# Kernel optimization log

Measured on AMD Instinct MI355X. Metric: run time of the kernel, lower is better.

The kernel has to match this reference:

```python
import jax, jax.numpy as jnp
import numpy as np

N, FIN, NH, NR, F, E = 50000, 256, 4, 4, 64, 500000


def setup_inputs() -> dict:
    key = jax.random.key(0)
    ks = jax.random.split(key, 12)
    x = jax.random.normal(ks[0], (N, FIN), jnp.float32)
    src = jax.random.randint(ks[1], (E,), 0, N)
    trg = jax.random.randint(ks[2], (E,), 0, N)
    rel = jax.random.randint(ks[3], (E,), 0, NR)
    node_to_graph_map = jnp.zeros((N,), jnp.int32)
    s = 1.0 / np.sqrt(FIN)
    W_proj = jax.random.uniform(ks[4], (NH * NR * F, FIN), jnp.float32, -s, s)
    score_src = jax.random.normal(ks[5], (1, NH, NR, F), jnp.float32) * 0.1
    score_trg = jax.random.normal(ks[6], (1, NH, NR, F), jnp.float32) * 0.1
    sf = 1.0 / np.sqrt(F)
    W1 = jax.random.uniform(ks[7], (F, F), jnp.float32, -sf, sf)
    b1 = jnp.zeros((F,), jnp.float32)
    W2 = jax.random.uniform(ks[8], (F, F), jnp.float32, -sf, sf)
    b2 = jnp.zeros((F,), jnp.float32)
    W3 = jax.random.uniform(ks[9], (1, F), jnp.float32, -sf, sf)
    b3 = jnp.zeros((1,), jnp.float32)
    W_skip = jax.random.uniform(ks[10], (NH * F, FIN), jnp.float32, -s, s)
    bias = jnp.zeros((NH * F,), jnp.float32)
    gamma = jnp.ones((NH * F,), jnp.float32)
    beta = jnp.zeros((NH * F,), jnp.float32)
    return dict(x=x, src=src, trg=trg, rel=rel, node_to_graph_map=node_to_graph_map,
                W_proj=W_proj, score_src=score_src, score_trg=score_trg,
                W1=W1, b1=b1, W2=W2, b2=b2, W3=W3, b3=b3,
                W_skip=W_skip, bias=bias, gamma=gamma, beta=beta)


def mish(v):
    return v * jnp.tanh(jax.nn.softplus(v))


def gat_forward(x, W_proj, score_src, score_trg, W1, b1, W2, b2, W3, b3,
                W_skip, bias, gamma, beta, src, trg, rel):
    n = x.shape[0]
    # (N, NH, NR, F) projected node features
    proj = (x @ W_proj.T).reshape(n, NH, NR, F)
    s_src = (proj * score_src).sum(-1)  # (N, NH, NR)
    s_trg = (proj * score_trg).sum(-1)  # (N, NH, NR)
    # lift to edges for their own relation: (E, NH)
    e_s = s_src[src, :, rel] + s_trg[trg, :, rel]
    e_s = jax.nn.leaky_relu(e_s, 0.2)
    # per-(relation, head) max over edges (matches per-relation max(dim=0) in the torch loop)
    m = jax.ops.segment_max(e_s, rel, num_segments=NR)  # (NR, NH)
    e_exp = jnp.exp(e_s - m[rel])
    # segment softmax grouped by (target node, relation)
    seg = trg * NR + rel
    denom = jax.ops.segment_sum(e_exp, seg, num_segments=n * NR)  # (N*NR, NH)
    att = e_exp / (denom[seg] + 1e-16)  # (E, NH)
    feat = proj[src, :, rel, :] * att[:, :, None]  # (E, NH, F)
    agg = jax.ops.segment_sum(feat, seg, num_segments=n * NR)  # (N*NR, NH, F)
    agg = agg.reshape(n, NR, NH, F).transpose(0, 2, 1, 3)  # (N, NH, NR, F)
    # AttentionedAggregationLayer: MLP score -> Mish -> softmax over relation dim -> weighted sum
    h = jax.nn.relu(agg @ W1.T + b1)
    h = jax.nn.relu(h @ W2.T + b2)
    sc = mish(h @ W3.T + b3)            # (N, NH, NR, 1)
    a_rel = jax.nn.softmax(sc, axis=-2)
    out = (agg * a_rel).sum(-2)          # (N, NH, F)
    # skip connection (FIN != NH*F per-head, so projected skip), concat heads, bias, ELU, LayerNorm
    out = out + (x @ W_skip.T).reshape(n, NH, F)
    out = out.reshape(n, NH * F) + bias
    out = jax.nn.elu(out)
    mu = out.mean(-1, keepdims=True)
    var = out.var(-1, keepdims=True)
    out = (out - mu) * jax.lax.rsqrt(var + 1e-5) * gamma + beta
    return out


def reference(x, src, trg, rel, node_to_graph_map, W_proj, score_src, score_trg,
              W1, b1, W2, b2, W3, b3, W_skip, bias, gamma, beta):
    return gat_forward(x, W_proj, score_src, score_trg, W1, b1, W2, b2, W3, b3,
                       W_skip, bias, gamma, beta, src, trg, rel)
```

## Files before the change

### kernel.cpp

```cpp
#include <hip/hip_runtime.h>

#define NNODES 50000
#define NEDGES 500000
#define NBINS  (NNODES * 4)
#define NSCANB 196
#define MPAD   50176

#define WF_W1    0
#define WF_B1    4096
#define WF_W2    4160
#define WF_B2    8256
#define WF_W3    8320
#define WF_B3    8384
#define WF_SSC   8388
#define WF_STC   9412
#define WF_BIAS  10436
#define WF_GAMMA 10692
#define WF_BETA  10948
#define WF_TOT   11204
#define WB_TOT   8192

typedef __attribute__((ext_vector_type(8))) short short8;
typedef __attribute__((ext_vector_type(4))) short short4v;
typedef __attribute__((ext_vector_type(4))) float floatx4;
typedef __attribute__((ext_vector_type(4))) unsigned int uint4v;

__device__ __forceinline__ float bf2f(unsigned short u) {
    return __uint_as_float(((unsigned)u) << 16);
}
__device__ __forceinline__ unsigned f2bf(float f) {
    unsigned u = __float_as_uint(f);
    u += 0x7fffu + ((u >> 16) & 1u);
    return u >> 16;
}
__device__ __forceinline__ int clampi(int v, int hi) { return v < 0 ? 0 : (v > hi ? hi : v); }

__global__ __launch_bounds__(256) void probe_k(const unsigned short* __restrict__ xs,
                                               unsigned* __restrict__ flag) {
    __shared__ unsigned cnt;
    if (threadIdx.x == 0) cnt = 0;
    __syncthreads();
    unsigned local = 0;
    for (int i = threadIdx.x; i < 8192; i += 256) {
        float v = bf2f(xs[i]);
        if (!(fabsf(v) < 1e10f)) local++;
    }
    atomicAdd(&cnt, local);
    __syncthreads();
    if (threadIdx.x == 0) *flag = (cnt > 256u) ? 1u : 0u;
}

__device__ __forceinline__ float ldf(const void* p, int i, bool f32) {
    return f32 ? ((const float*)p)[i] : bf2f(((const unsigned short*)p)[i]);
}

__global__ __launch_bounds__(1024) void wconv_k(const void* W1, const void* b1,
                                                const void* W2, const void* b2,
                                                const void* W3, const void* b3,
                                                const void* ssc, const void* stc,
                                                const void* bias, const void* gamma,
                                                const void* beta,
                                                const unsigned* __restrict__ flag,
                                                float* __restrict__ wf,
                                                unsigned short* __restrict__ wbf16) {
    bool f32 = (*flag != 0u);
    for (int i = threadIdx.x; i < WF_TOT + WB_TOT; i += 1024) {
        if (i >= WF_TOT) {
            int j = i - WF_TOT;
            float v = (j < 4096) ? ldf(W1, j, f32) : ldf(W2, j - 4096, f32);
            wbf16[j] = (unsigned short)f2bf(v);
            continue;
        }
        float v;
        if (i < WF_B1)          v = ldf(W1, i - WF_W1, f32);
        else if (i < WF_W2)     v = ldf(b1, i - WF_B1, f32);
        else if (i < WF_B2)     v = ldf(W2, i - WF_W2, f32);
        else if (i < WF_W3)     v = ldf(b2, i - WF_B2, f32);
        else if (i < WF_B3)     v = ldf(W3, i - WF_W3, f32);
        else if (i < WF_SSC) {
            int j = i - WF_B3;
            v = (j < 1) ? ldf(b3, j, f32) : 0.f;
        }
        else if (i < WF_STC)    v = ldf(ssc, i - WF_SSC, f32);
        else if (i < WF_BIAS)   v = ldf(stc, i - WF_STC, f32);
        else if (i < WF_GAMMA)  v = ldf(bias, i - WF_BIAS, f32);
        else if (i < WF_BETA)   v = ldf(gamma, i - WF_GAMMA, f32);
        else                    v = ldf(beta, i - WF_BETA, f32);
        wf[i] = v;
    }
}

__global__ __launch_bounds__(256) void convbf_k(const void* __restrict__ src,
                                                unsigned short* __restrict__ dst,
                                                int nelem, int npad,
                                                const unsigned* __restrict__ flag) {
    int i8 = (blockIdx.x * 256 + threadIdx.x) * 8;
    if (i8 >= npad) return;
    short8 o;
    if (i8 < nelem) {
        if (*flag) {
            const float* pf = (const float*)src + i8;
            floatx4 a = *(const floatx4*)pf;
            floatx4 b = *(const floatx4*)(pf + 4);
            o[0] = (short)f2bf(a[0]); o[1] = (short)f2bf(a[1]);
            o[2] = (short)f2bf(a[2]); o[3] = (short)f2bf(a[3]);
            o[4] = (short)f2bf(b[0]); o[5] = (short)f2bf(b[1]);
            o[6] = (short)f2bf(b[2]); o[7] = (short)f2bf(b[3]);
        } else {
            o = *(const short8*)((const unsigned short*)src + i8);
        }
    } else {
#pragma unroll
        for (int j = 0; j < 8; j++) o[j] = 0;
    }
    *(short8*)(dst + i8) = o;
}

__global__ __launch_bounds__(64) void gemm_fused_k(const unsigned short* __restrict__ A,
                                                   const unsigned short* __restrict__ Bp,
                                                   const unsigned short* __restrict__ Bs,
                                                   unsigned short* __restrict__ proj,
                                                   unsigned short* __restrict__ out16,
                                                   float* __restrict__ out32,
                                                   const float* __restrict__ wf,
                                                   float* __restrict__ s_src,
                                                   float* __restrict__ s_trg,
                                                   const unsigned* __restrict__ flag) {
    const bool cf32 = (*flag != 0u);
    const int lane = threadIdx.x & 63;
    const int l15 = lane & 15, q = lane >> 4;
    const int m0 = blockIdx.x * 64;
    const int cg0 = blockIdx.y * 4;

    short8 af[4][8];
#pragma unroll
    for (int mt = 0; mt < 4; mt++)
#pragma unroll
        for (int ks = 0; ks < 8; ks++)
            af[mt][ks] = *(const short8*)(A + (size_t)(m0 + mt * 16 + l15) * 256 + ks * 32 + q * 8);

    if (cg0 < 16) {
#pragma unroll 1
        for (int cgi = 0; cgi < 4; cgi++) {
            const int cg = cg0 + cgi;
            floatx4 acc[4][4];
#pragma unroll
            for (int i = 0; i < 4; i++)
#pragma unroll
                for (int j = 0; j < 4; j++) acc[i][j] = (floatx4){0.f, 0.f, 0.f, 0.f};
#pragma unroll
            for (int ks = 0; ks < 8; ks++) {
                short8 bfr[4];
#pragma unroll
                for (int nt = 0; nt < 4; nt++)
                    bfr[nt] = *(const short8*)(Bp + (size_t)(cg * 64 + nt * 16 + l15) * 256 + ks * 32 + q * 8);
#pragma unroll
                for (int mt = 0; mt < 4; mt++)
#pragma unroll
                    for (int nt = 0; nt < 4; nt++)
                        acc[mt][nt] = __builtin_amdgcn_mfma_f32_16x16x32_bf16(bfr[nt], af[mt][ks],
                                                                             acc[mt][nt], 0, 0, 0);
            }
            const int h = cg >> 2, r = cg & 3;
            const int colbase = (r * 4 + h) * 64;
            const int cell = r * 4 + h;
            const int scell = h * 4 + r;
            floatx4 sa4[4], sb4[4];
#pragma unroll
            for (int nt = 0; nt < 4; nt++) {
                sa4[nt] = *(const floatx4*)(wf + WF_SSC + scell * 64 + nt * 16 + q * 4);
                sb4[nt] = *(const floatx4*)(wf + WF_STC + scell * 64 + nt * 16 + q * 4);
            }
#pragma unroll
            for (int mt = 0; mt < 4; mt++) {
                const int row = m0 + mt * 16 + l15;
                float pa = 0.f, pb = 0.f;
#pragma unroll
                for (int nt = 0; nt < 4; nt++) {
                    short4v sv;
#pragma unroll
                    for (int rg = 0; rg < 4; rg++) {
                        float v = acc[mt][nt][rg];
                        unsigned short vb = (unsigned short)f2bf(v);
                        sv[rg] = (short)vb;
                        float vr = bf2f(vb);
                        pa = fmaf(vr, sa4[nt][rg], pa);
                        pb = fmaf(vr, sb4[nt][rg], pb);
                    }
                    if (row < NNODES)
                        *(short4v*)(proj + (size_t)row * 1024 + colbase + nt * 16 + q * 4) = sv;
                }
                pa += __shfl_xor(pa, 16);
                pa += __shfl_xor(pa, 32);
                pb += __shfl_xor(pb, 16);
                pb += __shfl_xor(pb, 32);
                if (q == 0 && row < NNODES) {
                    s_src[row * 16 + cell] = pa;
                    s_trg[row * 16 + cell] = pb;
                }
            }
        }
    } else {
#pragma unroll 1
        for (int cg = 0; cg < 4; cg++) {
            floatx4 acc[4][4];
#pragma unroll
            for (int i = 0; i < 4; i++)
#pragma unroll
                for (int j = 0; j < 4; j++) acc[i][j] = (floatx4){0.f, 0.f, 0.f, 0.f};
#pragma unroll
            for (int ks = 0; ks < 8; ks++) {
                short8 bfr[4];
#pragma unroll
                for (int nt = 0; nt < 4; nt++)
                    bfr[nt] = *(const short8*)(Bs + (size_t)(cg * 64 + nt * 16 + l15) * 256 + ks * 32 + q * 8);
#pragma unroll
                for (int mt = 0; mt < 4; mt++)
#pragma unroll
                    for (int nt = 0; nt < 4; nt++)
                        acc[mt][nt] = __builtin_amdgcn_mfma_f32_16x16x32_bf16(bfr[nt], af[mt][ks],
                                                                             acc[mt][nt], 0, 0, 0);
            }
#pragma unroll
            for (int mt = 0; mt < 4; mt++) {
                const int row = m0 + mt * 16 + l15;
                if (row >= NNODES) continue;
#pragma unroll
                for (int nt = 0; nt < 4; nt++) {
                    if (cf32) {
                        floatx4 o = acc[mt][nt];
                        *(floatx4*)(out32 + (size_t)row * 256 + cg * 64 + nt * 16 + q * 4) = o;
                    } else {
                        short4v sv;
#pragma unroll
                        for (int rg = 0; rg < 4; rg++)
                            sv[rg] = (short)f2bf(acc[mt][nt][rg]);
                        *(short4v*)(out16 + (size_t)row * 256 + cg * 64 + nt * 16 + q * 4) = sv;
                    }
                }
            }
        }
    }
}

__global__ __launch_bounds__(256) void count_k(const int* __restrict__ trg,
                                               const int* __restrict__ rel,
                                               unsigned* __restrict__ counts, int E) {
    int e = blockIdx.x * 256 + threadIdx.x;
    if (e >= E) return;
    int g = clampi(trg[e], NNODES - 1);
    int r = clampi(rel[e], 3);
    atomicAdd(&counts[g * 4 + r], 1u);
}

__global__ __launch_bounds__(256) void scan1_k(const unsigned* __restrict__ counts,
                                               unsigned* __restrict__ offsets,
                                               unsigned* __restrict__ bsum) {
    __shared__ unsigned ts[256];
    int t = threadIdx.x;
    int base = blockIdx.x * 1024 + t * 4;
    uint4v c = {0u, 0u, 0u, 0u};
    if (base + 3 < NBINS) c = *(const uint4v*)(counts + base);
    else {
#pragma unroll
        for (int j = 0; j < 4; j++) c[j] = (base + j < NBINS) ? counts[base + j] : 0u;
    }
    ts[t] = c[0] + c[1] + c[2] + c[3];
    __syncthreads();
    for (int off = 1; off < 256; off <<= 1) {
        unsigned v = (t >= off) ? ts[t - off] : 0u;
        __syncthreads();
        ts[t] += v;
        __syncthreads();
    }
    unsigned pre = (t == 0) ? 0u : ts[t - 1];
    uint4v o;
    o[0] = pre;
    o[1] = pre + c[0];
    o[2] = pre + c[0] + c[1];
    o[3] = pre + c[0] + c[1] + c[2];
    if (base + 3 < NBINS) *(uint4v*)(offsets + base) = o;
    else {
#pragma unroll
        for (int j = 0; j < 4; j++) if (base + j < NBINS) offsets[base + j] = o[j];
    }
    if (t == 255) bsum[blockIdx.x] = ts[255];
}

__global__ __launch_bounds__(256) void scan2_k(unsigned* __restrict__ bsum,
                                               unsigned* __restrict__ offsets) {
    __shared__ unsigned ts[256];
    int t = threadIdx.x;
    unsigned v = (t < NSCANB) ? bsum[t] : 0u;
    ts[t] = v;
    __syncthreads();
    for (int off = 1; off < 256; off <<= 1) {
        unsigned u = (t >= off) ? ts[t - off] : 0u;
        __syncthreads();
        ts[t] += u;
        __syncthreads();
    }
    if (t < NSCANB) bsum[t] = (t == 0) ? 0u : ts[t - 1];
    if (t == 255) offsets[NBINS] = ts[255];
}

__global__ __launch_bounds__(256) void scan3_k(unsigned* __restrict__ offsets,
                                               unsigned* __restrict__ cursor,
                                               const unsigned* __restrict__ bsum) {
    int t = threadIdx.x;
    unsigned base = bsum[blockIdx.x];
    int idx = blockIdx.x * 1024 + t * 4;
    if (idx + 3 < NBINS) {
        uint4v o = *(const uint4v*)(offsets + idx);
        o[0] += base; o[1] += base; o[2] += base; o[3] += base;
        *(uint4v*)(offsets + idx) = o;
        *(uint4v*)(cursor + idx) = o;
    } else {
#pragma unroll
        for (int j = 0; j < 4; j++)
            if (idx + j < NBINS) {
                unsigned v = offsets[idx + j] + base;
                offsets[idx + j] = v;
                cursor[idx + j] = v;
            }
    }
}

__global__ __launch_bounds__(256) void fill_k(const int* __restrict__ src,
                                              const int* __restrict__ trg,
                                              const int* __restrict__ rel,
                                              const float* __restrict__ s_src,
                                              const float* __restrict__ s_trg,
                                              unsigned* __restrict__ cursor,
                                              unsigned* __restrict__ esrc,
                                              floatx4* __restrict__ eexp, int E) {
    int e = blockIdx.x * 256 + threadIdx.x;
    if (e >= E) return;
    int s = clampi(src[e], NNODES - 1);
    int g = clampi(trg[e], NNODES - 1);
    int r = clampi(rel[e], 3);
    unsigned pos = atomicAdd(&cursor[g * 4 + r], 1u);
    if (pos >= (unsigned)E) pos = E - 1;
    esrc[pos] = (unsigned)s;
    floatx4 aa = *(const floatx4*)(s_src + s * 16 + r * 4);
    floatx4 bb = *(const floatx4*)(s_trg + g * 16 + r * 4);
    floatx4 v;
#pragma unroll
    for (int h = 0; h < 4; h++) {
        float val = aa[h] + bb[h];
        val = val > 0.f ? val : 0.2f * val;
        v[h] = expf(val);
    }
    eexp[pos] = v;
}

__device__ __forceinline__ void edge_acc(const unsigned* esrc, const floatx4* eexp,
                                         const unsigned short* proj, int r, int h,
                                         int lane, unsigned beg, unsigned end,
                                         float* a, float* den) {
    unsigned i = beg;
    for (; i + 2 <= end; i += 2) {
        unsigned s0 = esrc[i], s1 = esrc[i + 1];
        floatx4 pe0 = eexp[i], pe1 = eexp[i + 1];
        short4v v0 = *((const short4v*)(proj + (size_t)s0 * 1024 + r * 256) + lane);
        short4v v1 = *((const short4v*)(proj + (size_t)s1 * 1024 + r * 256) + lane);
        float p0 = pe0[h], p1 = pe1[h];
        *den += p0 + p1;
        a[0] = fmaf(p0, bf2f((unsigned short)v0[0]), a[0]);
        a[1] = fmaf(p0, bf2f((unsigned short)v0[1]), a[1]);
        a[2] = fmaf(p0, bf2f((unsigned short)v0[2]), a[2]);
        a[3] = fmaf(p0, bf2f((unsigned short)v0[3]), a[3]);
        a[0] = fmaf(p1, bf2f((unsigned short)v1[0]), a[0]);
        a[1] = fmaf(p1, bf2f((unsigned short)v1[1]), a[1]);
        a[2] = fmaf(p1, bf2f((unsigned short)v1[2]), a[2]);
        a[3] = fmaf(p1, bf2f((unsigned short)v1[3]), a[3]);
    }
    if (i < end) {
        unsigned s0 = esrc[i];
        floatx4 pe0 = eexp[i];
        short4v v0 = *((const short4v*)(proj + (size_t)s0 * 1024 + r * 256) + lane);
        float p0 = pe0[h];
        *den += p0;
        a[0] = fmaf(p0, bf2f((unsigned short)v0[0]), a[0]);
        a[1] = fmaf(p0, bf2f((unsigned short)v0[1]), a[1]);
        a[2] = fmaf(p0, bf2f((unsigned short)v0[2]), a[2]);
        a[3] = fmaf(p0, bf2f((unsigned short)v0[3]), a[3]);
    }
}

__global__ __launch_bounds__(256) void node_fused_k(const unsigned* __restrict__ offsets,
                                                    const unsigned* __restrict__ esrc,
                                                    const floatx4* __restrict__ eexp,
                                                    const unsigned short* __restrict__ proj,
                                                    const unsigned short* __restrict__ wbf16,
                                                    const float* __restrict__ wf,
                                                    const unsigned* __restrict__ flag,
                                                    unsigned short* __restrict__ out16,
                                                    float* __restrict__ out32) {
    __shared__ unsigned short aggL[4][16 * 72];
    __shared__ float hidL[4][16 * 68];
    const bool f32 = (*flag != 0u);
    const int wave = threadIdx.x >> 6;
    const int lane = threadIdx.x & 63;
    const int l15 = lane & 15, q = lane >> 4;
    unsigned short* aL = aggL[wave];
    float* hL = hidL[wave];

    short8 w1f[2][4], w2f[2][4];
#pragma unroll
    for (int ks = 0; ks < 2; ks++)
#pragma unroll
        for (int nt = 0; nt < 4; nt++) {
            w1f[ks][nt] = *(const short8*)(wbf16 + (nt * 16 + l15) * 64 + ks * 32 + q * 8);
            w2f[ks][nt] = *(const short8*)(wbf16 + 4096 + (nt * 16 + l15) * 64 + ks * 32 + q * 8);
        }
    float b1v[4], b2v[4], w3v[4];
#pragma unroll
    for (int nt = 0; nt < 4; nt++) {
        b1v[nt] = wf[WF_B1 + nt * 16 + l15];
        b2v[nt] = wf[WF_B2 + nt * 16 + l15];
        w3v[nt] = wf[WF_W3 + nt * 16 + l15];
    }
    const float b3v = wf[WF_B3];

    const int c0 = q * 64 + l15 * 4;
    const floatx4 bi = *(const floatx4*)(wf + WF_BIAS + c0);
    const floatx4 ga = *(const floatx4*)(wf + WF_GAMMA + c0);
    const floatx4 be = *(const floatx4*)(wf + WF_BETA + c0);

    const int n = blockIdx.x * 4 + wave;

#pragma unroll
    for (int r = 0; r < 4; r++) {
        const int bin = n * 4 + r;
        unsigned beg = offsets[bin], end = offsets[bin + 1];
        float a[4] = {0.f, 0.f, 0.f, 0.f};
        float den = 0.f;
        edge_acc(esrc, eexp, proj, r, q, lane, beg, end, a, &den);
        float inv = 1.f / (den + 1e-16f);
        short4v o;
        o[0] = (short)f2bf(a[0] * inv);
        o[1] = (short)f2bf(a[1] * inv);
        o[2] = (short)f2bf(a[2] * inv);
        o[3] = (short)f2bf(a[3] * inv);
        *(short4v*)(aL + (r * 4 + q) * 72 + l15 * 4) = o;
    }

    short8 a1[2];
#pragma unroll
    for (int ks = 0; ks < 2; ks++)
        a1[ks] = *(const short8*)(aL + l15 * 72 + ks * 32 + q * 8);
    floatx4 acc1[4];
#pragma unroll
    for (int nt = 0; nt < 4; nt++) {
        acc1[nt] = (floatx4){0.f, 0.f, 0.f, 0.f};
        acc1[nt] = __builtin_amdgcn_mfma_f32_16x16x32_bf16(a1[0], w1f[0][nt], acc1[nt], 0, 0, 0);
        acc1[nt] = __builtin_amdgcn_mfma_f32_16x16x32_bf16(a1[1], w1f[1][nt], acc1[nt], 0, 0, 0);
    }
#pragma unroll
    for (int nt = 0; nt < 4; nt++)
#pragma unroll
        for (int rg = 0; rg < 4; rg++)
            hL[(q * 4 + rg) * 68 + nt * 16 + l15] = fmaxf(acc1[nt][rg] + b1v[nt], 0.f);
    short8 a2[2];
#pragma unroll
    for (int ks = 0; ks < 2; ks++) {
        short8 rr;
#pragma unroll
        for (int j = 0; j < 8; j++)
            rr[j] = (short)f2bf(hL[l15 * 68 + ks * 32 + q * 8 + j]);
        a2[ks] = rr;
    }
    floatx4 acc2[4];
#pragma unroll
    for (int nt = 0; nt < 4; nt++) {
        acc2[nt] = (floatx4){0.f, 0.f, 0.f, 0.f};
        acc2[nt] = __builtin_amdgcn_mfma_f32_16x16x32_bf16(a2[0], w2f[0][nt], acc2[nt], 0, 0, 0);
        acc2[nt] = __builtin_amdgcn_mfma_f32_16x16x32_bf16(a2[1], w2f[1][nt], acc2[nt], 0, 0, 0);
    }
    float p[4];
#pragma unroll
    for (int rg = 0; rg < 4; rg++) {
        float s = 0.f;
#pragma unroll
        for (int nt = 0; nt < 4; nt++)
            s = fmaf(fmaxf(acc2[nt][rg] + b2v[nt], 0.f), w3v[nt], s);
        p[rg] = s;
    }
#pragma unroll
    for (int off = 1; off < 16; off <<= 1) {
#pragma unroll
        for (int rg = 0; rg < 4; rg++) p[rg] += __shfl_xor(p[rg], off);
    }
    float psel = (l15 & 2) ? ((l15 & 1) ? p[3] : p[2])
                           : ((l15 & 1) ? p[1] : p[0]);
    float acc = psel + b3v;
    float sp = fmaxf(acc, 0.f) + log1pf(expf(-fabsf(acc)));
    float msh = acc * tanhf(sp);

    float sv0 = __shfl(msh, 0 * 16 + q);
    float sv1 = __shfl(msh, 1 * 16 + q);
    float sv2 = __shfl(msh, 2 * 16 + q);
    float sv3 = __shfl(msh, 3 * 16 + q);
    float mx = fmaxf(fmaxf(sv0, sv1), fmaxf(sv2, sv3));
    float e0 = expf(sv0 - mx), e1 = expf(sv1 - mx);
    float e2 = expf(sv2 - mx), e3 = expf(sv3 - mx);
    float inv = 1.f / (e0 + e1 + e2 + e3);
    float er[4] = {e0 * inv, e1 * inv, e2 * inv, e3 * inv};

    float acc4[4] = {0.f, 0.f, 0.f, 0.f};
#pragma unroll
    for (int r = 0; r < 4; r++) {
        short4v av = *(const short4v*)(aL + (r * 4 + q) * 72 + l15 * 4);
        float e = er[r];
        acc4[0] = fmaf(e, bf2f((unsigned short)av[0]), acc4[0]);
        acc4[1] = fmaf(e, bf2f((unsigned short)av[1]), acc4[1]);
        acc4[2] = fmaf(e, bf2f((unsigned short)av[2]), acc4[2]);
        acc4[3] = fmaf(e, bf2f((unsigned short)av[3]), acc4[3]);
    }

    const size_t ob = (size_t)n * 256 + c0;
    float v[4];
    if (f32) {
        floatx4 sk = *(const floatx4*)(out32 + ob);
#pragma unroll
        for (int j = 0; j < 4; j++) v[j] = acc4[j] + sk[j] + bi[j];
    } else {
        short4v sk = *(const short4v*)(out16 + ob);
#pragma unroll
        for (int j = 0; j < 4; j++) v[j] = acc4[j] + bf2f((unsigned short)sk[j]) + bi[j];
    }
#pragma unroll
    for (int j = 0; j < 4; j++) v[j] = v[j] > 0.f ? v[j] : expm1f(v[j]);

    float s = v[0] + v[1] + v[2] + v[3];
    float qq = v[0] * v[0] + v[1] * v[1] + v[2] * v[2] + v[3] * v[3];
#pragma unroll
    for (int o = 1; o < 64; o <<= 1) {
        s += __shfl_xor(s, o);
        qq += __shfl_xor(qq, o);
    }
    float mu = s * (1.f / 256.f);
    float var = fmaxf(qq * (1.f / 256.f) - mu * mu, 0.f);
    float rstd = rsqrtf(var + 1e-5f);

    if (f32) {
        floatx4 o4v;
#pragma unroll
        for (int j = 0; j < 4; j++) o4v[j] = (v[j] - mu) * rstd * ga[j] + be[j];
        *(floatx4*)(out32 + ob) = o4v;
    } else {
        short4v o4v;
#pragma unroll
        for (int j = 0; j < 4; j++) o4v[j] = (short)f2bf((v[j] - mu) * rstd * ga[j] + be[j]);
        *(short4v*)(out16 + ob) = o4v;
    }
}

extern "C" void kernel_launch(void* const* d_in, const int* in_sizes, int n_in,
                              void* d_out, int out_size, void* d_ws, size_t ws_size,
                              hipStream_t stream) {
    if (ws_size < 226900000) return;

    const void* x      = d_in[0];
    const int* src     = (const int*)d_in[1];
    const int* trg     = (const int*)d_in[2];
    const int* rel     = (const int*)d_in[3];
    const void* W_proj = d_in[5];
    const void* ssc    = d_in[6];
    const void* stc    = d_in[7];
    const void* W1     = d_in[8];
    const void* b1     = d_in[9];
    const void* W2     = d_in[10];
    const void* b2     = d_in[11];
    const void* W3     = d_in[12];
    const void* b3     = d_in[13];
    const void* W_skip = d_in[14];
    const void* bias   = d_in[15];
    const void* gamma  = d_in[16];
    const void* beta   = d_in[17];
    unsigned short* out16 = (unsigned short*)d_out;
    float* out32          = (float*)d_out;

    char* w = (char*)d_ws;
    unsigned short* proj = (unsigned short*)(w + 0);
    unsigned short* xbf  = (unsigned short*)(w + 102400000);
    float* s_src         = (float*)(w + 204800000);
    float* s_trg         = (float*)(w + 208000000);
    floatx4* eexp        = (floatx4*)(w + 211200000);
    unsigned short* wpbf = (unsigned short*)(w + 211200000);
    unsigned short* wsbf = (unsigned short*)(w + 212300000);
    unsigned* esrc       = (unsigned*)(w + 219200000);
    unsigned* counts     = (unsigned*)(w + 221200000);
    unsigned* offsets    = (unsigned*)(w + 222000000);
    unsigned* cursor     = (unsigned*)(w + 222800016);
    float* wf            = (float*)(w + 226800016);
    unsigned short* wbf16= (unsigned short*)(w + 226844832);
    unsigned* flag       = (unsigned*)(w + 226861216);
    unsigned* bsum       = (unsigned*)(w + 226861224);

    hipMemsetAsync(counts, 0, NBINS * 4, stream);

    probe_k<<<1, 256, 0, stream>>>((const unsigned short*)x, flag);
    wconv_k<<<1, 1024, 0, stream>>>(W1, b1, W2, b2, W3, b3, ssc, stc, bias, gamma, beta,
                                    flag, wf, wbf16);
    convbf_k<<<(MPAD * 256) / (8 * 256), 256, 0, stream>>>(x, xbf, NNODES * 256,
                                                           MPAD * 256, flag);
    convbf_k<<<128, 256, 0, stream>>>(W_proj, wpbf, 1024 * 256, 1024 * 256, flag);
    convbf_k<<<32, 256, 0, stream>>>(W_skip, wsbf, 256 * 256, 256 * 256, flag);
    gemm_fused_k<<<dim3(784, 5), 64, 0, stream>>>(xbf, wpbf, wsbf, proj, out16, out32,
                                                  wf, s_src, s_trg, flag);
    count_k<<<1954, 256, 0, stream>>>(trg, rel, counts, NEDGES);
    scan1_k<<<NSCANB, 256, 0, stream>>>(counts, offsets, bsum);
    scan2_k<<<1, 256, 0, stream>>>(bsum, offsets);
    scan3_k<<<NSCANB, 256, 0, stream>>>(offsets, cursor, bsum);
    fill_k<<<1954, 256, 0, stream>>>(src, trg, rel, s_src, s_trg, cursor, esrc, eexp, NEDGES);
    node_fused_k<<<12500, 256, 0, stream>>>(offsets, esrc, eexp, proj, wbf16, wf, flag,
                                            out16, out32);
}
```

Baseline: 564.3 us.

## Process four relations in parallel per wave and loop four nodes per wave

The edge gather in node_fused_k is restructured. Instead of one relation at a time with every lane loading 4 bf16 features, each 16-lane quarter now handles one relation and each lane loads 16 contiguous features with two 16-byte loads. The loop runs under __any with masked inactive lanes. Each wave also loops over 4 nodes, so the grid shrinks by a factor of four and the hoisted weight fragments are reused across nodes. The trade-off is more divergence when relation bins have uneven edge counts, higher register pressure from 16 accumulators, and fewer blocks to hide gather latency.

```diff
diff --git a/kernel.cpp b/kernel.cpp
--- a/kernel.cpp
+++ b/kernel.cpp
@@ -354,40 +354,6 @@
     eexp[pos] = v;
 }
 
-__device__ __forceinline__ void edge_acc(const unsigned* esrc, const floatx4* eexp,
-                                         const unsigned short* proj, int r, int h,
-                                         int lane, unsigned beg, unsigned end,
-                                         float* a, float* den) {
-    unsigned i = beg;
-    for (; i + 2 <= end; i += 2) {
-        unsigned s0 = esrc[i], s1 = esrc[i + 1];
-        floatx4 pe0 = eexp[i], pe1 = eexp[i + 1];
-        short4v v0 = *((const short4v*)(proj + (size_t)s0 * 1024 + r * 256) + lane);
-        short4v v1 = *((const short4v*)(proj + (size_t)s1 * 1024 + r * 256) + lane);
-        float p0 = pe0[h], p1 = pe1[h];
-        *den += p0 + p1;
-        a[0] = fmaf(p0, bf2f((unsigned short)v0[0]), a[0]);
-        a[1] = fmaf(p0, bf2f((unsigned short)v0[1]), a[1]);
-        a[2] = fmaf(p0, bf2f((unsigned short)v0[2]), a[2]);
-        a[3] = fmaf(p0, bf2f((unsigned short)v0[3]), a[3]);
-        a[0] = fmaf(p1, bf2f((unsigned short)v1[0]), a[0]);
-        a[1] = fmaf(p1, bf2f((unsigned short)v1[1]), a[1]);
-        a[2] = fmaf(p1, bf2f((unsigned short)v1[2]), a[2]);
-        a[3] = fmaf(p1, bf2f((unsigned short)v1[3]), a[3]);
-    }
-    if (i < end) {
-        unsigned s0 = esrc[i];
-        floatx4 pe0 = eexp[i];
-        short4v v0 = *((const short4v*)(proj + (size_t)s0 * 1024 + r * 256) + lane);
-        float p0 = pe0[h];
-        *den += p0;
-        a[0] = fmaf(p0, bf2f((unsigned short)v0[0]), a[0]);
-        a[1] = fmaf(p0, bf2f((unsigned short)v0[1]), a[1]);
-        a[2] = fmaf(p0, bf2f((unsigned short)v0[2]), a[2]);
-        a[3] = fmaf(p0, bf2f((unsigned short)v0[3]), a[3]);
-    }
-}
-
 __global__ __launch_bounds__(256) void node_fused_k(const unsigned* __restrict__ offsets,
                                                     const unsigned* __restrict__ esrc,
                                                     const floatx4* __restrict__ eexp,
@@ -428,132 +394,160 @@
     const floatx4 ga = *(const floatx4*)(wf + WF_GAMMA + c0);
     const floatx4 be = *(const floatx4*)(wf + WF_BETA + c0);
 
-    const int n = blockIdx.x * 4 + wave;
-
-#pragma unroll
-    for (int r = 0; r < 4; r++) {
-        const int bin = n * 4 + r;
-        unsigned beg = offsets[bin], end = offsets[bin + 1];
-        float a[4] = {0.f, 0.f, 0.f, 0.f};
-        float den = 0.f;
-        edge_acc(esrc, eexp, proj, r, q, lane, beg, end, a, &den);
-        float inv = 1.f / (den + 1e-16f);
-        short4v o;
-        o[0] = (short)f2bf(a[0] * inv);
-        o[1] = (short)f2bf(a[1] * inv);
-        o[2] = (short)f2bf(a[2] * inv);
-        o[3] = (short)f2bf(a[3] * inv);
-        *(short4v*)(aL + (r * 4 + q) * 72 + l15 * 4) = o;
-    }
-
-    short8 a1[2];
-#pragma unroll
-    for (int ks = 0; ks < 2; ks++)
-        a1[ks] = *(const short8*)(aL + l15 * 72 + ks * 32 + q * 8);
-    floatx4 acc1[4];
-#pragma unroll
-    for (int nt = 0; nt < 4; nt++) {
-        acc1[nt] = (floatx4){0.f, 0.f, 0.f, 0.f};
-        acc1[nt] = __builtin_amdgcn_mfma_f32_16x16x32_bf16(a1[0], w1f[0][nt], acc1[nt], 0, 0, 0);
-        acc1[nt] = __builtin_amdgcn_mfma_f32_16x16x32_bf16(a1[1], w1f[1][nt], acc1[nt], 0, 0, 0);
-    }
-#pragma unroll
-    for (int nt = 0; nt < 4; nt++)
-#pragma unroll
-        for (int rg = 0; rg < 4; rg++)
-            hL[(q * 4 + rg) * 68 + nt * 16 + l15] = fmaxf(acc1[nt][rg] + b1v[nt], 0.f);
-    short8 a2[2];
-#pragma unroll
-    for (int ks = 0; ks < 2; ks++) {
-        short8 rr;
-#pragma unroll
-        for (int j = 0; j < 8; j++)
-            rr[j] = (short)f2bf(hL[l15 * 68 + ks * 32 + q * 8 + j]);
-        a2[ks] = rr;
-    }
-    floatx4 acc2[4];
-#pragma unroll
-    for (int nt = 0; nt < 4; nt++) {
-        acc2[nt] = (floatx4){0.f, 0.f, 0.f, 0.f};
-        acc2[nt] = __builtin_amdgcn_mfma_f32_16x16x32_bf16(a2[0], w2f[0][nt], acc2[nt], 0, 0, 0);
-        acc2[nt] = __builtin_amdgcn_mfma_f32_16x16x32_bf16(a2[1], w2f[1][nt], acc2[nt], 0, 0, 0);
-    }
-    float p[4];
-#pragma unroll
-    for (int rg = 0; rg < 4; rg++) {
-        float s = 0.f;
+    const int wave_id = blockIdx.x * 4 + wave;
+#pragma unroll 1
+    for (int t = 0; t < 4; t++) {
+        const int n = wave_id * 4 + t;
+
+        {
+            const int g = q;
+            const int j = l15;
+            const int hh = j >> 2;
+            unsigned i = offsets[n * 4 + g];
+            const unsigned end = offsets[n * 4 + g + 1];
+            float a[16];
+#pragma unroll
+            for (int k = 0; k < 16; k++) a[k] = 0.f;
+            float den = 0.f;
+            while (__any(i < end)) {
+                const bool act = i < end;
+                const unsigned ii = act ? i : 0u;
+                unsigned s0 = esrc[ii];
+                floatx4 pe = eexp[ii];
+                const unsigned short* pp = proj + (size_t)s0 * 1024 + g * 256 + j * 16;
+                short8 v0 = *(const short8*)(pp);
+                short8 v1 = *(const short8*)(pp + 8);
+                float p = act ? pe[hh] : 0.f;
+                den += p;
+#pragma unroll
+                for (int k = 0; k < 8; k++)
+                    a[k] = fmaf(p, bf2f((unsigned short)v0[k]), a[k]);
+#pragma unroll
+                for (int k = 0; k < 8; k++)
+                    a[8 + k] = fmaf(p, bf2f((unsigned short)v1[k]), a[8 + k]);
+                if (act) i++;
+            }
+            float inv = 1.f / (den + 1e-16f);
+            unsigned short* dst = aL + (g * 4 + hh) * 72 + (j & 3) * 16;
+            short8 o0, o1;
+#pragma unroll
+            for (int k = 0; k < 8; k++) {
+                o0[k] = (short)f2bf(a[k] * inv);
+                o1[k] = (short)f2bf(a[8 + k] * inv);
+            }
+            *(short8*)(dst) = o0;
+            *(short8*)(dst + 8) = o1;
+        }
+
+        short8 a1[2];
+#pragma unroll
+        for (int ks = 0; ks < 2; ks++)
+            a1[ks] = *(const short8*)(aL + l15 * 72 + ks * 32 + q * 8);
+        floatx4 acc1[4];
+#pragma unroll
+        for (int nt = 0; nt < 4; nt++) {
+            acc1[nt] = (floatx4){0.f, 0.f, 0.f, 0.f};
+            acc1[nt] = __builtin_amdgcn_mfma_f32_16x16x32_bf16(a1[0], w1f[0][nt], acc1[nt], 0, 0, 0);
+            acc1[nt] = __builtin_amdgcn_mfma_f32_16x16x32_bf16(a1[1], w1f[1][nt], acc1[nt], 0, 0, 0);
+        }
 #pragma unroll
         for (int nt = 0; nt < 4; nt++)
-            s = fmaf(fmaxf(acc2[nt][rg] + b2v[nt], 0.f), w3v[nt], s);
-        p[rg] = s;
-    }
-#pragma unroll
-    for (int off = 1; off < 16; off <<= 1) {
-#pragma unroll
-        for (int rg = 0; rg < 4; rg++) p[rg] += __shfl_xor(p[rg], off);
-    }
-    float psel = (l15 & 2) ? ((l15 & 1) ? p[3] : p[2])
-                           : ((l15 & 1) ? p[1] : p[0]);
-    float acc = psel + b3v;
-    float sp = fmaxf(acc, 0.f) + log1pf(expf(-fabsf(acc)));
-    float msh = acc * tanhf(sp);
-
-    float sv0 = __shfl(msh, 0 * 16 + q);
-    float sv1 = __shfl(msh, 1 * 16 + q);
-    float sv2 = __shfl(msh, 2 * 16 + q);
-    float sv3 = __shfl(msh, 3 * 16 + q);
-    float mx = fmaxf(fmaxf(sv0, sv1), fmaxf(sv2, sv3));
-    float e0 = expf(sv0 - mx), e1 = expf(sv1 - mx);
-    float e2 = expf(sv2 - mx), e3 = expf(sv3 - mx);
-    float inv = 1.f / (e0 + e1 + e2 + e3);
-    float er[4] = {e0 * inv, e1 * inv, e2 * inv, e3 * inv};
-
-    float acc4[4] = {0.f, 0.f, 0.f, 0.f};
-#pragma unroll
-    for (int r = 0; r < 4; r++) {
-        short4v av = *(const short4v*)(aL + (r * 4 + q) * 72 + l15 * 4);
-        float e = er[r];
-        acc4[0] = fmaf(e, bf2f((unsigned short)av[0]), acc4[0]);
-        acc4[1] = fmaf(e, bf2f((unsigned short)av[1]), acc4[1]);
-        acc4[2] = fmaf(e, bf2f((unsigned short)av[2]), acc4[2]);
-        acc4[3] = fmaf(e, bf2f((unsigned short)av[3]), acc4[3]);
-    }
-
-    const size_t ob = (size_t)n * 256 + c0;
-    float v[4];
-    if (f32) {
-        floatx4 sk = *(const floatx4*)(out32 + ob);
-#pragma unroll
-        for (int j = 0; j < 4; j++) v[j] = acc4[j] + sk[j] + bi[j];
-    } else {
-        short4v sk = *(const short4v*)(out16 + ob);
-#pragma unroll
-        for (int j = 0; j < 4; j++) v[j] = acc4[j] + bf2f((unsigned short)sk[j]) + bi[j];
-    }
-#pragma unroll
-    for (int j = 0; j < 4; j++) v[j] = v[j] > 0.f ? v[j] : expm1f(v[j]);
-
-    float s = v[0] + v[1] + v[2] + v[3];
-    float qq = v[0] * v[0] + v[1] * v[1] + v[2] * v[2] + v[3] * v[3];
-#pragma unroll
-    for (int o = 1; o < 64; o <<= 1) {
-        s += __shfl_xor(s, o);
-        qq += __shfl_xor(qq, o);
-    }
-    float mu = s * (1.f / 256.f);
-    float var = fmaxf(qq * (1.f / 256.f) - mu * mu, 0.f);
-    float rstd = rsqrtf(var + 1e-5f);
-
-    if (f32) {
-        floatx4 o4v;
-#pragma unroll
-        for (int j = 0; j < 4; j++) o4v[j] = (v[j] - mu) * rstd * ga[j] + be[j];
-        *(floatx4*)(out32 + ob) = o4v;
-    } else {
-        short4v o4v;
-#pragma unroll
-        for (int j = 0; j < 4; j++) o4v[j] = (short)f2bf((v[j] - mu) * rstd * ga[j] + be[j]);
-        *(short4v*)(out16 + ob) = o4v;
+#pragma unroll
+            for (int rg = 0; rg < 4; rg++)
+                hL[(q * 4 + rg) * 68 + nt * 16 + l15] = fmaxf(acc1[nt][rg] + b1v[nt], 0.f);
+        short8 a2[2];
+#pragma unroll
+        for (int ks = 0; ks < 2; ks++) {
+            short8 rr;
+#pragma unroll
+            for (int jx = 0; jx < 8; jx++)
+                rr[jx] = (short)f2bf(hL[l15 * 68 + ks * 32 + q * 8 + jx]);
+            a2[ks] = rr;
+        }
+        floatx4 acc2[4];
+#pragma unroll
+        for (int nt = 0; nt < 4; nt++) {
+            acc2[nt] = (floatx4){0.f, 0.f, 0.f, 0.f};
+            acc2[nt] = __builtin_amdgcn_mfma_f32_16x16x32_bf16(a2[0], w2f[0][nt], acc2[nt], 0, 0, 0);
+            acc2[nt] = __builtin_amdgcn_mfma_f32_16x16x32_bf16(a2[1], w2f[1][nt], acc2[nt], 0, 0, 0);
+        }
+        float p[4];
+#pragma unroll
+        for (int rg = 0; rg < 4; rg++) {
+            float s = 0.f;
+#pragma unroll
+            for (int nt = 0; nt < 4; nt++)
+                s = fmaf(fmaxf(acc2[nt][rg] + b2v[nt], 0.f), w3v[nt], s);
+            p[rg] = s;
+        }
+#pragma unroll
+        for (int off = 1; off < 16; off <<= 1) {
+#pragma unroll
+            for (int rg = 0; rg < 4; rg++) p[rg] += __shfl_xor(p[rg], off);
+        }
+        float psel = (l15 & 2) ? ((l15 & 1) ? p[3] : p[2])
+                               : ((l15 & 1) ? p[1] : p[0]);
+        float acc = psel + b3v;
+        float sp = fmaxf(acc, 0.f) + log1pf(expf(-fabsf(acc)));
+        float msh = acc * tanhf(sp);
+
+        float sv0 = __shfl(msh, 0 * 16 + q);
+        float sv1 = __shfl(msh, 1 * 16 + q);
+        float sv2 = __shfl(msh, 2 * 16 + q);
+        float sv3 = __shfl(msh, 3 * 16 + q);
+        float mx = fmaxf(fmaxf(sv0, sv1), fmaxf(sv2, sv3));
+        float e0 = expf(sv0 - mx), e1 = expf(sv1 - mx);
+        float e2 = expf(sv2 - mx), e3 = expf(sv3 - mx);
+        float inv = 1.f / (e0 + e1 + e2 + e3);
+        float er[4] = {e0 * inv, e1 * inv, e2 * inv, e3 * inv};
+
+        float acc4[4] = {0.f, 0.f, 0.f, 0.f};
+#pragma unroll
+        for (int r = 0; r < 4; r++) {
+            short4v av = *(const short4v*)(aL + (r * 4 + q) * 72 + l15 * 4);
+            float e = er[r];
+            acc4[0] = fmaf(e, bf2f((unsigned short)av[0]), acc4[0]);
+            acc4[1] = fmaf(e, bf2f((unsigned short)av[1]), acc4[1]);
+            acc4[2] = fmaf(e, bf2f((unsigned short)av[2]), acc4[2]);
+            acc4[3] = fmaf(e, bf2f((unsigned short)av[3]), acc4[3]);
+        }
+
+        const size_t ob = (size_t)n * 256 + c0;
+        float v[4];
+        if (f32) {
+            floatx4 sk = *(const floatx4*)(out32 + ob);
+#pragma unroll
+            for (int jx = 0; jx < 4; jx++) v[jx] = acc4[jx] + sk[jx] + bi[jx];
+        } else {
+            short4v sk = *(const short4v*)(out16 + ob);
+#pragma unroll
+            for (int jx = 0; jx < 4; jx++) v[jx] = acc4[jx] + bf2f((unsigned short)sk[jx]) + bi[jx];
+        }
+#pragma unroll
+        for (int jx = 0; jx < 4; jx++) v[jx] = v[jx] > 0.f ? v[jx] : expm1f(v[jx]);
+
+        float s = v[0] + v[1] + v[2] + v[3];
+        float qq = v[0] * v[0] + v[1] * v[1] + v[2] * v[2] + v[3] * v[3];
+#pragma unroll
+        for (int o = 1; o < 64; o <<= 1) {
+            s += __shfl_xor(s, o);
+            qq += __shfl_xor(qq, o);
+        }
+        float mu = s * (1.f / 256.f);
+        float var = fmaxf(qq * (1.f / 256.f) - mu * mu, 0.f);
+        float rstd = rsqrtf(var + 1e-5f);
+
+        if (f32) {
+            floatx4 o4v;
+#pragma unroll
+            for (int jx = 0; jx < 4; jx++) o4v[jx] = (v[jx] - mu) * rstd * ga[jx] + be[jx];
+            *(floatx4*)(out32 + ob) = o4v;
+        } else {
+            short4v o4v;
+#pragma unroll
+            for (int jx = 0; jx < 4; jx++) o4v[jx] = (short)f2bf((v[jx] - mu) * rstd * ga[jx] + be[jx]);
+            *(short4v*)(out16 + ob) = o4v;
+        }
     }
 }
 
@@ -615,6 +609,6 @@
     scan2_k<<<1, 256, 0, stream>>>(bsum, offsets);
     scan3_k<<<NSCANB, 256, 0, stream>>>(offsets, cursor, bsum);
     fill_k<<<1954, 256, 0, stream>>>(src, trg, rel, s_src, s_trg, cursor, esrc, eexp, NEDGES);
-    node_fused_k<<<12500, 256, 0, stream>>>(offsets, esrc, eexp, proj, wbf16, wf, flag,
-                                            out16, out32);
-}
+    node_fused_k<<<3125, 256, 0, stream>>>(offsets, esrc, eexp, proj, wbf16, wf, flag,
+                                           out16, out32);
+}
```

Measured after the change: 526.3 us. -6.7%, faster.

## Merge dtype probe into weight conversion, halve GEMM row tile, loop nodes per wave

Applied to the files above, without the earlier changes.

Folds the input-dtype probe kernel into the weight-conversion kernel, removing one launch. The projection GEMM now uses 32-row tiles instead of 64, doubling the grid and cutting accumulator and A-fragment registers. The aim is better occupancy and load balance. The node kernel now makes each wave handle four nodes in a loop, with a quarter of the blocks, so the per-wave weight-fragment setup is amortized. The trade-offs are less B-tile reuse in the GEMM and less parallelism in the node stage.

```diff
diff --git a/kernel.cpp b/kernel.cpp
--- a/kernel.cpp
+++ b/kernel.cpp
@@ -35,35 +35,33 @@
 }
 __device__ __forceinline__ int clampi(int v, int hi) { return v < 0 ? 0 : (v > hi ? hi : v); }
 
-__global__ __launch_bounds__(256) void probe_k(const unsigned short* __restrict__ xs,
-                                               unsigned* __restrict__ flag) {
-    __shared__ unsigned cnt;
-    if (threadIdx.x == 0) cnt = 0;
-    __syncthreads();
-    unsigned local = 0;
-    for (int i = threadIdx.x; i < 8192; i += 256) {
-        float v = bf2f(xs[i]);
-        if (!(fabsf(v) < 1e10f)) local++;
-    }
-    atomicAdd(&cnt, local);
-    __syncthreads();
-    if (threadIdx.x == 0) *flag = (cnt > 256u) ? 1u : 0u;
-}
-
 __device__ __forceinline__ float ldf(const void* p, int i, bool f32) {
     return f32 ? ((const float*)p)[i] : bf2f(((const unsigned short*)p)[i]);
 }
 
-__global__ __launch_bounds__(1024) void wconv_k(const void* W1, const void* b1,
+__global__ __launch_bounds__(1024) void wconv_k(const unsigned short* __restrict__ xs,
+                                                const void* W1, const void* b1,
                                                 const void* W2, const void* b2,
                                                 const void* W3, const void* b3,
                                                 const void* ssc, const void* stc,
                                                 const void* bias, const void* gamma,
                                                 const void* beta,
-                                                const unsigned* __restrict__ flag,
+                                                unsigned* __restrict__ flag,
                                                 float* __restrict__ wf,
                                                 unsigned short* __restrict__ wbf16) {
-    bool f32 = (*flag != 0u);
+    __shared__ unsigned cnt;
+    if (threadIdx.x == 0) cnt = 0;
+    __syncthreads();
+    unsigned local = 0;
+    for (int i = threadIdx.x; i < 8192; i += 1024) {
+        float v = bf2f(xs[i]);
+        if (!(fabsf(v) < 1e10f)) local++;
+    }
+    atomicAdd(&cnt, local);
+    __syncthreads();
+    const bool f32 = (cnt > 256u);
+    if (threadIdx.x == 0) *flag = f32 ? 1u : 0u;
+
     for (int i = threadIdx.x; i < WF_TOT + WB_TOT; i += 1024) {
         if (i >= WF_TOT) {
             int j = i - WF_TOT;
@@ -129,12 +127,12 @@
     const bool cf32 = (*flag != 0u);
     const int lane = threadIdx.x & 63;
     const int l15 = lane & 15, q = lane >> 4;
-    const int m0 = blockIdx.x * 64;
+    const int m0 = blockIdx.x * 32;
     const int cg0 = blockIdx.y * 4;
 
-    short8 af[4][8];
-#pragma unroll
-    for (int mt = 0; mt < 4; mt++)
+    short8 af[2][8];
+#pragma unroll
+    for (int mt = 0; mt < 2; mt++)
 #pragma unroll
         for (int ks = 0; ks < 8; ks++)
             af[mt][ks] = *(const short8*)(A + (size_t)(m0 + mt * 16 + l15) * 256 + ks * 32 + q * 8);
@@ -143,9 +141,9 @@
 #pragma unroll 1
         for (int cgi = 0; cgi < 4; cgi++) {
             const int cg = cg0 + cgi;
-            floatx4 acc[4][4];
-#pragma unroll
-            for (int i = 0; i < 4; i++)
+            floatx4 acc[2][4];
+#pragma unroll
+            for (int i = 0; i < 2; i++)
 #pragma unroll
                 for (int j = 0; j < 4; j++) acc[i][j] = (floatx4){0.f, 0.f, 0.f, 0.f};
 #pragma unroll
@@ -155,7 +153,7 @@
                 for (int nt = 0; nt < 4; nt++)
                     bfr[nt] = *(const short8*)(Bp + (size_t)(cg * 64 + nt * 16 + l15) * 256 + ks * 32 + q * 8);
 #pragma unroll
-                for (int mt = 0; mt < 4; mt++)
+                for (int mt = 0; mt < 2; mt++)
 #pragma unroll
                     for (int nt = 0; nt < 4; nt++)
                         acc[mt][nt] = __builtin_amdgcn_mfma_f32_16x16x32_bf16(bfr[nt], af[mt][ks],
@@ -172,7 +170,7 @@
                 sb4[nt] = *(const floatx4*)(wf + WF_STC + scell * 64 + nt * 16 + q * 4);
             }
 #pragma unroll
-            for (int mt = 0; mt < 4; mt++) {
+            for (int mt = 0; mt < 2; mt++) {
                 const int row = m0 + mt * 16 + l15;
                 float pa = 0.f, pb = 0.f;
 #pragma unroll
@@ -203,9 +201,9 @@
     } else {
 #pragma unroll 1
         for (int cg = 0; cg < 4; cg++) {
-            floatx4 acc[4][4];
-#pragma unroll
-            for (int i = 0; i < 4; i++)
+            floatx4 acc[2][4];
+#pragma unroll
+            for (int i = 0; i < 2; i++)
 #pragma unroll
                 for (int j = 0; j < 4; j++) acc[i][j] = (floatx4){0.f, 0.f, 0.f, 0.f};
 #pragma unroll
@@ -215,14 +213,14 @@
                 for (int nt = 0; nt < 4; nt++)
                     bfr[nt] = *(const short8*)(Bs + (size_t)(cg * 64 + nt * 16 + l15) * 256 + ks * 32 + q * 8);
 #pragma unroll
-                for (int mt = 0; mt < 4; mt++)
+                for (int mt = 0; mt < 2; mt++)
 #pragma unroll
                     for (int nt = 0; nt < 4; nt++)
                         acc[mt][nt] = __builtin_amdgcn_mfma_f32_16x16x32_bf16(bfr[nt], af[mt][ks],
                                                                              acc[mt][nt], 0, 0, 0);
             }
 #pragma unroll
-            for (int mt = 0; mt < 4; mt++) {
+            for (int mt = 0; mt < 2; mt++) {
                 const int row = m0 + mt * 16 + l15;
                 if (row >= NNODES) continue;
 #pragma unroll
@@ -428,132 +426,136 @@
     const floatx4 ga = *(const floatx4*)(wf + WF_GAMMA + c0);
     const floatx4 be = *(const floatx4*)(wf + WF_BETA + c0);
 
-    const int n = blockIdx.x * 4 + wave;
-
-#pragma unroll
-    for (int r = 0; r < 4; r++) {
-        const int bin = n * 4 + r;
-        unsigned beg = offsets[bin], end = offsets[bin + 1];
-        float a[4] = {0.f, 0.f, 0.f, 0.f};
-        float den = 0.f;
-        edge_acc(esrc, eexp, proj, r, q, lane, beg, end, a, &den);
-        float inv = 1.f / (den + 1e-16f);
-        short4v o;
-        o[0] = (short)f2bf(a[0] * inv);
-        o[1] = (short)f2bf(a[1] * inv);
-        o[2] = (short)f2bf(a[2] * inv);
-        o[3] = (short)f2bf(a[3] * inv);
-        *(short4v*)(aL + (r * 4 + q) * 72 + l15 * 4) = o;
-    }
-
-    short8 a1[2];
-#pragma unroll
-    for (int ks = 0; ks < 2; ks++)
-        a1[ks] = *(const short8*)(aL + l15 * 72 + ks * 32 + q * 8);
-    floatx4 acc1[4];
-#pragma unroll
-    for (int nt = 0; nt < 4; nt++) {
-        acc1[nt] = (floatx4){0.f, 0.f, 0.f, 0.f};
-        acc1[nt] = __builtin_amdgcn_mfma_f32_16x16x32_bf16(a1[0], w1f[0][nt], acc1[nt], 0, 0, 0);
-        acc1[nt] = __builtin_amdgcn_mfma_f32_16x16x32_bf16(a1[1], w1f[1][nt], acc1[nt], 0, 0, 0);
-    }
-#pragma unroll
-    for (int nt = 0; nt < 4; nt++)
-#pragma unroll
-        for (int rg = 0; rg < 4; rg++)
-            hL[(q * 4 + rg) * 68 + nt * 16 + l15] = fmaxf(acc1[nt][rg] + b1v[nt], 0.f);
-    short8 a2[2];
-#pragma unroll
-    for (int ks = 0; ks < 2; ks++) {
-        short8 rr;
-#pragma unroll
-        for (int j = 0; j < 8; j++)
-            rr[j] = (short)f2bf(hL[l15 * 68 + ks * 32 + q * 8 + j]);
-        a2[ks] = rr;
-    }
-    floatx4 acc2[4];
-#pragma unroll
-    for (int nt = 0; nt < 4; nt++) {
-        acc2[nt] = (floatx4){0.f, 0.f, 0.f, 0.f};
-        acc2[nt] = __builtin_amdgcn_mfma_f32_16x16x32_bf16(a2[0], w2f[0][nt], acc2[nt], 0, 0, 0);
-        acc2[nt] = __builtin_amdgcn_mfma_f32_16x16x32_bf16(a2[1], w2f[1][nt], acc2[nt], 0, 0, 0);
-    }
-    float p[4];
-#pragma unroll
-    for (int rg = 0; rg < 4; rg++) {
-        float s = 0.f;
+    const int wave_id = blockIdx.x * 4 + wave;
+#pragma unroll 1
+    for (int t = 0; t < 4; t++) {
+        const int n = wave_id * 4 + t;
+
+#pragma unroll
+        for (int r = 0; r < 4; r++) {
+            const int bin = n * 4 + r;
+            unsigned beg = offsets[bin], end = offsets[bin + 1];
+            float a[4] = {0.f, 0.f, 0.f, 0.f};
+            float den = 0.f;
+            edge_acc(esrc, eexp, proj, r, q, lane, beg, end, a, &den);
+            float inv = 1.f / (den + 1e-16f);
+            short4v o;
+            o[0] = (short)f2bf(a[0] * inv);
+            o[1] = (short)f2bf(a[1] * inv);
+            o[2] = (short)f2bf(a[2] * inv);
+            o[3] = (short)f2bf(a[3] * inv);
+            *(short4v*)(aL + (r * 4 + q) * 72 + l15 * 4) = o;
+        }
+
+        short8 a1[2];
+#pragma unroll
+        for (int ks = 0; ks < 2; ks++)
+            a1[ks] = *(const short8*)(aL + l15 * 72 + ks * 32 + q * 8);
+        floatx4 acc1[4];
+#pragma unroll
+        for (int nt = 0; nt < 4; nt++) {
+            acc1[nt] = (floatx4){0.f, 0.f, 0.f, 0.f};
+            acc1[nt] = __builtin_amdgcn_mfma_f32_16x16x32_bf16(a1[0], w1f[0][nt], acc1[nt], 0, 0, 0);
+            acc1[nt] = __builtin_amdgcn_mfma_f32_16x16x32_bf16(a1[1], w1f[1][nt], acc1[nt], 0, 0, 0);
+        }
 #pragma unroll
         for (int nt = 0; nt < 4; nt++)
-            s = fmaf(fmaxf(acc2[nt][rg] + b2v[nt], 0.f), w3v[nt], s);
-        p[rg] = s;
-    }
-#pragma unroll
-    for (int off = 1; off < 16; off <<= 1) {
-#pragma unroll
-        for (int rg = 0; rg < 4; rg++) p[rg] += __shfl_xor(p[rg], off);
-    }
-    float psel = (l15 & 2) ? ((l15 & 1) ? p[3] : p[2])
-                           : ((l15 & 1) ? p[1] : p[0]);
-    float acc = psel + b3v;
-    float sp = fmaxf(acc, 0.f) + log1pf(expf(-fabsf(acc)));
-    float msh = acc * tanhf(sp);
-
-    float sv0 = __shfl(msh, 0 * 16 + q);
-    float sv1 = __shfl(msh, 1 * 16 + q);
-    float sv2 = __shfl(msh, 2 * 16 + q);
-    float sv3 = __shfl(msh, 3 * 16 + q);
-    float mx = fmaxf(fmaxf(sv0, sv1), fmaxf(sv2, sv3));
-    float e0 = expf(sv0 - mx), e1 = expf(sv1 - mx);
-    float e2 = expf(sv2 - mx), e3 = expf(sv3 - mx);
-    float inv = 1.f / (e0 + e1 + e2 + e3);
-    float er[4] = {e0 * inv, e1 * inv, e2 * inv, e3 * inv};
-
-    float acc4[4] = {0.f, 0.f, 0.f, 0.f};
-#pragma unroll
-    for (int r = 0; r < 4; r++) {
-        short4v av = *(const short4v*)(aL + (r * 4 + q) * 72 + l15 * 4);
-        float e = er[r];
-        acc4[0] = fmaf(e, bf2f((unsigned short)av[0]), acc4[0]);
-        acc4[1] = fmaf(e, bf2f((unsigned short)av[1]), acc4[1]);
-        acc4[2] = fmaf(e, bf2f((unsigned short)av[2]), acc4[2]);
-        acc4[3] = fmaf(e, bf2f((unsigned short)av[3]), acc4[3]);
-    }
-
-    const size_t ob = (size_t)n * 256 + c0;
-    float v[4];
-    if (f32) {
-        floatx4 sk = *(const floatx4*)(out32 + ob);
-#pragma unroll
-        for (int j = 0; j < 4; j++) v[j] = acc4[j] + sk[j] + bi[j];
-    } else {
-        short4v sk = *(const short4v*)(out16 + ob);
-#pragma unroll
-        for (int j = 0; j < 4; j++) v[j] = acc4[j] + bf2f((unsigned short)sk[j]) + bi[j];
-    }
-#pragma unroll
-    for (int j = 0; j < 4; j++) v[j] = v[j] > 0.f ? v[j] : expm1f(v[j]);
-
-    float s = v[0] + v[1] + v[2] + v[3];
-    float qq = v[0] * v[0] + v[1] * v[1] + v[2] * v[2] + v[3] * v[3];
-#pragma unroll
-    for (int o = 1; o < 64; o <<= 1) {
-        s += __shfl_xor(s, o);
-        qq += __shfl_xor(qq, o);
-    }
-    float mu = s * (1.f / 256.f);
-    float var = fmaxf(qq * (1.f / 256.f) - mu * mu, 0.f);
-    float rstd = rsqrtf(var + 1e-5f);
-
-    if (f32) {
-        floatx4 o4v;
-#pragma unroll
-        for (int j = 0; j < 4; j++) o4v[j] = (v[j] - mu) * rstd * ga[j] + be[j];
-        *(floatx4*)(out32 + ob) = o4v;
-    } else {
-        short4v o4v;
-#pragma unroll
-        for (int j = 0; j < 4; j++) o4v[j] = (short)f2bf((v[j] - mu) * rstd * ga[j] + be[j]);
-        *(short4v*)(out16 + ob) = o4v;
+#pragma unroll
+            for (int rg = 0; rg < 4; rg++)
+                hL[(q * 4 + rg) * 68 + nt * 16 + l15] = fmaxf(acc1[nt][rg] + b1v[nt], 0.f);
+        short8 a2[2];
+#pragma unroll
+        for (int ks = 0; ks < 2; ks++) {
+            short8 rr;
+#pragma unroll
+            for (int jx = 0; jx < 8; jx++)
+                rr[jx] = (short)f2bf(hL[l15 * 68 + ks * 32 + q * 8 + jx]);
+            a2[ks] = rr;
+        }
+        floatx4 acc2[4];
+#pragma unroll
+        for (int nt = 0; nt < 4; nt++) {
+            acc2[nt] = (floatx4){0.f, 0.f, 0.f, 0.f};
+            acc2[nt] = __builtin_amdgcn_mfma_f32_16x16x32_bf16(a2[0], w2f[0][nt], acc2[nt], 0, 0, 0);
+            acc2[nt] = __builtin_amdgcn_mfma_f32_16x16x32_bf16(a2[1], w2f[1][nt], acc2[nt], 0, 0, 0);
+        }
+        float p[4];
+#pragma unroll
+        for (int rg = 0; rg < 4; rg++) {
+            float s = 0.f;
+#pragma unroll
+            for (int nt = 0; nt < 4; nt++)
+                s = fmaf(fmaxf(acc2[nt][rg] + b2v[nt], 0.f), w3v[nt], s);
+            p[rg] = s;
+        }
+#pragma unroll
+        for (int off = 1; off < 16; off <<= 1) {
+#pragma unroll
+            for (int rg = 0; rg < 4; rg++) p[rg] += __shfl_xor(p[rg], off);
+        }
+        float psel = (l15 & 2) ? ((l15 & 1) ? p[3] : p[2])
+                               : ((l15 & 1) ? p[1] : p[0]);
+        float acc = psel + b3v;
+        float sp = fmaxf(acc, 0.f) + log1pf(expf(-fabsf(acc)));
+        float msh = acc * tanhf(sp);
+
+        float sv0 = __shfl(msh, 0 * 16 + q);
+        float sv1 = __shfl(msh, 1 * 16 + q);
+        float sv2 = __shfl(msh, 2 * 16 + q);
+        float sv3 = __shfl(msh, 3 * 16 + q);
+        float mx = fmaxf(fmaxf(sv0, sv1), fmaxf(sv2, sv3));
+        float e0 = expf(sv0 - mx), e1 = expf(sv1 - mx);
+        float e2 = expf(sv2 - mx), e3 = expf(sv3 - mx);
+        float inv = 1.f / (e0 + e1 + e2 + e3);
+        float er[4] = {e0 * inv, e1 * inv, e2 * inv, e3 * inv};
+
+        float acc4[4] = {0.f, 0.f, 0.f, 0.f};
+#pragma unroll
+        for (int r = 0; r < 4; r++) {
+            short4v av = *(const short4v*)(aL + (r * 4 + q) * 72 + l15 * 4);
+            float e = er[r];
+            acc4[0] = fmaf(e, bf2f((unsigned short)av[0]), acc4[0]);
+            acc4[1] = fmaf(e, bf2f((unsigned short)av[1]), acc4[1]);
+            acc4[2] = fmaf(e, bf2f((unsigned short)av[2]), acc4[2]);
+            acc4[3] = fmaf(e, bf2f((unsigned short)av[3]), acc4[3]);
+        }
+
+        const size_t ob = (size_t)n * 256 + c0;
+        float v[4];
+        if (f32) {
+            floatx4 sk = *(const floatx4*)(out32 + ob);
+#pragma unroll
+            for (int jx = 0; jx < 4; jx++) v[jx] = acc4[jx] + sk[jx] + bi[jx];
+        } else {
+            short4v sk = *(const short4v*)(out16 + ob);
+#pragma unroll
+            for (int jx = 0; jx < 4; jx++) v[jx] = acc4[jx] + bf2f((unsigned short)sk[jx]) + bi[jx];
+        }
+#pragma unroll
+        for (int jx = 0; jx < 4; jx++) v[jx] = v[jx] > 0.f ? v[jx] : expm1f(v[jx]);
+
+        float s = v[0] + v[1] + v[2] + v[3];
+        float qq = v[0] * v[0] + v[1] * v[1] + v[2] * v[2] + v[3] * v[3];
+#pragma unroll
+        for (int o = 1; o < 64; o <<= 1) {
+            s += __shfl_xor(s, o);
+            qq += __shfl_xor(qq, o);
+        }
+        float mu = s * (1.f / 256.f);
+        float var = fmaxf(qq * (1.f / 256.f) - mu * mu, 0.f);
+        float rstd = rsqrtf(var + 1e-5f);
+
+        if (f32) {
+            floatx4 o4v;
+#pragma unroll
+            for (int jx = 0; jx < 4; jx++) o4v[jx] = (v[jx] - mu) * rstd * ga[jx] + be[jx];
+            *(floatx4*)(out32 + ob) = o4v;
+        } else {
+            short4v o4v;
+#pragma unroll
+            for (int jx = 0; jx < 4; jx++) o4v[jx] = (short)f2bf((v[jx] - mu) * rstd * ga[jx] + be[jx]);
+            *(short4v*)(out16 + ob) = o4v;
+        }
     }
 }
 
@@ -601,20 +603,19 @@
 
     hipMemsetAsync(counts, 0, NBINS * 4, stream);
 
-    probe_k<<<1, 256, 0, stream>>>((const unsigned short*)x, flag);
-    wconv_k<<<1, 1024, 0, stream>>>(W1, b1, W2, b2, W3, b3, ssc, stc, bias, gamma, beta,
-                                    flag, wf, wbf16);
+    wconv_k<<<1, 1024, 0, stream>>>((const unsigned short*)x, W1, b1, W2, b2, W3, b3,
+                                    ssc, stc, bias, gamma, beta, flag, wf, wbf16);
     convbf_k<<<(MPAD * 256) / (8 * 256), 256, 0, stream>>>(x, xbf, NNODES * 256,
                                                            MPAD * 256, flag);
     convbf_k<<<128, 256, 0, stream>>>(W_proj, wpbf, 1024 * 256, 1024 * 256, flag);
     convbf_k<<<32, 256, 0, stream>>>(W_skip, wsbf, 256 * 256, 256 * 256, flag);
-    gemm_fused_k<<<dim3(784, 5), 64, 0, stream>>>(xbf, wpbf, wsbf, proj, out16, out32,
-                                                  wf, s_src, s_trg, flag);
+    gemm_fused_k<<<dim3(1568, 5), 64, 0, stream>>>(xbf, wpbf, wsbf, proj, out16, out32,
+                                                   wf, s_src, s_trg, flag);
     count_k<<<1954, 256, 0, stream>>>(trg, rel, counts, NEDGES);
     scan1_k<<<NSCANB, 256, 0, stream>>>(counts, offsets, bsum);
     scan2_k<<<1, 256, 0, stream>>>(bsum, offsets);
     scan3_k<<<NSCANB, 256, 0, stream>>>(offsets, cursor, bsum);
     fill_k<<<1954, 256, 0, stream>>>(src, trg, rel, s_src, s_trg, cursor, esrc, eexp, NEDGES);
-    node_fused_k<<<12500, 256, 0, stream>>>(offsets, esrc, eexp, proj, wbf16, wf, flag,
-                                            out16, out32);
-}
+    node_fused_k<<<3125, 256, 0, stream>>>(offsets, esrc, eexp, proj, wbf16, wf, flag,
+                                           out16, out32);
+}
```

After: 535.6 us. 5.1% less time.
